# Optimization experiments

Measured on AMD Instinct MI355X. Metric: run time of the kernel, lower is better.

The kernel has to match this reference:

```python
import jax, jax.numpy as jnp
import numpy as np
from jax import lax

TOPK = 10
THRESHOLD = 0.5
MARGIN = 0.5
EPS = 1e-8


def setup_inputs() -> dict:
    key = jax.random.key(0)
    k1, k2 = jax.random.split(key)
    B, C, H, W = 8, 256, 128, 128
    loc_features = jax.random.normal(k1, (B, C, H, W), dtype=jnp.float32)
    det_features = jax.random.normal(k2, (B, C, H, W), dtype=jnp.float32)
    return {"loc_features": loc_features, "det_features": det_features}


def _peak_features(fmap):
    """fmap: [C,H,W] -> (feats [TOPK,C], valid [TOPK] bool).
    Peaks = pixels equal to their 3x3 local max with intensity > THRESHOLD,
    sorted by intensity descending, top TOPK (padded with invalid slots)."""
    C, H, W = fmap.shape
    intensity = jnp.sqrt(jnp.sum(fmap * fmap, axis=0))  # [H,W] L2 norm over channels
    pooled = lax.reduce_window(intensity, -jnp.inf, lax.max,
                               (3, 3), (1, 1), 'SAME')
    peak_mask = (intensity == pooled) & (intensity > THRESHOLD)
    masked = jnp.where(peak_mask, intensity, -jnp.inf).reshape(-1)  # [H*W]
    vals, idx = lax.top_k(masked, TOPK)
    valid = jnp.isfinite(vals)  # slots beyond the actual peak count are -inf
    y = idx // W
    x = idx % W
    feats = fmap[:, y, x].T  # [TOPK, C]
    return feats, valid


def _cosine_sim(a, b):
    # a: [Ka,C], b: [Kb,C]; torch.cosine_similarity semantics with eps clamp
    na = jnp.maximum(jnp.linalg.norm(a, axis=-1), EPS)  # [Ka]
    nb = jnp.maximum(jnp.linalg.norm(b, axis=-1), EPS)  # [Kb]
    return (a @ b.T) / (na[:, None] * nb[None, :])


def _per_sample_loss(det_map, loc_map):
    det_f, det_v = _peak_features(det_map)
    loc_f, loc_v = _peak_features(loc_map)
    sim = _cosine_sim(det_f, loc_f)  # [TOPK, TOPK]
    pair_mask = det_v[:, None] & loc_v[None, :]
    n_pairs = jnp.sum(pair_mask)
    loss_sum = jnp.sum(jnp.where(pair_mask, jax.nn.relu(sim - MARGIN), 0.0))
    # torch 'continue' when either side has no peaks -> contributes 0
    return jnp.where(n_pairs > 0, loss_sum / jnp.maximum(n_pairs, 1).astype(sim.dtype), 0.0)


def reference(loc_features, det_features):
    B = loc_features.shape[0]
    losses = jax.vmap(_per_sample_loss)(det_features, loc_features)  # [B]
    return jnp.sum(losses) / B
```

## Files before the change

### kernel.cpp

```cpp
#include <hip/hip_runtime.h>
#include <math.h>

namespace {
constexpr int kB = 8;
constexpr int kC = 256;
constexpr int kH = 128;
constexpr int kW = 128;
constexpr int kHW = kH * kW;
constexpr int kTopK = 10;
constexpr float kThreshold = 0.5f;
constexpr float kMargin = 0.5f;
constexpr float kEps = 1e-8f;
constexpr int kMaps = 2 * kB;
constexpr int kGrpPlanes = 16;
constexpr int kGroups = kC / kGrpPlanes;
constexpr int kQuarter = kHW / 4;
constexpr int kBands = 16;
constexpr int kBandRows = kH / kBands;
}

__global__ __launch_bounds__(512, 4) void sumsq_kernel(
    const float* __restrict__ loc, const float* __restrict__ det,
    float* __restrict__ partial) {
  const int bid = blockIdx.x;
  const int m = bid >> 6;
  const int g = (bid >> 2) & 15;
  const int q = bid & 3;
  const int t = threadIdx.x;
  const float* __restrict__ src = (m < kB) ? loc : det;
  const int b = m & (kB - 1);
  const float* base = src + (size_t)b * kC * kHW +
                      (size_t)(g * kGrpPlanes) * kHW + q * kQuarter + t * 4;
  float4 a0 = {0.f, 0.f, 0.f, 0.f};
  float4 a1 = {0.f, 0.f, 0.f, 0.f};
  for (int j = 0; j < kGrpPlanes; j += 8) {
    float4 v[16];
#pragma unroll
    for (int jj = 0; jj < 8; ++jj) {
      const float* pb = base + (size_t)(j + jj) * kHW;
      v[2 * jj] = *(const float4*)pb;
      v[2 * jj + 1] = *(const float4*)(pb + 2048);
    }
    __builtin_amdgcn_sched_barrier(0);
#pragma unroll
    for (int jj = 0; jj < 8; ++jj) {
      const float4 u = v[2 * jj];
      const float4 x = v[2 * jj + 1];
      a0.x = fmaf(u.x, u.x, a0.x);
      a0.y = fmaf(u.y, u.y, a0.y);
      a0.z = fmaf(u.z, u.z, a0.z);
      a0.w = fmaf(u.w, u.w, a0.w);
      a1.x = fmaf(x.x, x.x, a1.x);
      a1.y = fmaf(x.y, x.y, a1.y);
      a1.z = fmaf(x.z, x.z, a1.z);
      a1.w = fmaf(x.w, x.w, a1.w);
    }
  }
  float* out = partial + ((size_t)m * kGroups + g) * kHW + q * kQuarter + t * 4;
  *(float4*)out = a0;
  *(float4*)(out + 2048) = a1;
}

__global__ __launch_bounds__(256) void peaktop_kernel(
    const float* __restrict__ partial, float* __restrict__ cvals,
    int* __restrict__ cidx) {
  const int m = blockIdx.x >> 4;
  const int band = blockIdx.x & 15;
  const int r0 = band * kBandRows;
  const int t = threadIdx.x;
  const int w = t >> 6;
  const int lane = t & 63;
  __shared__ float ld[kBandRows + 2][kW + 4];
  __shared__ float swv[4][kTopK];
  __shared__ int swi[4][kTopK];

  const int prow0 = r0 - 1;
  float acc[5] = {0.f, 0.f, 0.f, 0.f, 0.f};
  const float* pbase = partial + (size_t)m * kGroups * kHW + prow0 * kW;
#pragma unroll 4
  for (int g = 0; g < kGroups; ++g) {
    const float* pg = pbase + (size_t)g * kHW;
#pragma unroll
    for (int i = 0; i < 5; ++i) {
      const int p = t + 256 * i;
      const int gr = prow0 + (p >> 7);
      if (gr >= 0 && gr < kH) acc[i] += pg[p];
    }
  }
#pragma unroll
  for (int i = 0; i < 5; ++i) {
    const int p = t + 256 * i;
    const int gr = prow0 + (p >> 7);
    ld[p >> 7][p & 127] = (gr >= 0 && gr < kH) ? sqrtf(acc[i]) : -INFINITY;
  }
  __syncthreads();

  float cv[4];
  int ci[4];
#pragma unroll
  for (int i = 0; i < 4; ++i) {
    const int op = t + 256 * i;
    const int tr = (op >> 7) + 1;
    const int col = op & 127;
    const float c0 = ld[tr][col];
    float nmax = -INFINITY;
#pragma unroll
    for (int dy = -1; dy <= 1; ++dy) {
#pragma unroll
      for (int dx = -1; dx <= 1; ++dx) {
        const int xx = col + dx;
        if (xx >= 0 && xx < kW) nmax = fmaxf(nmax, ld[tr + dy][xx]);
      }
    }
    const bool peak = (c0 > kThreshold) && (c0 >= nmax);
    cv[i] = peak ? c0 : -INFINITY;
    ci[i] = (r0 + (op >> 7)) * kW + col;
  }

  for (int r = 0; r < kTopK; ++r) {
    float bv = cv[0];
    int bi = ci[0];
#pragma unroll
    for (int i = 1; i < 4; ++i)
      if (cv[i] > bv || (cv[i] == bv && ci[i] < bi)) { bv = cv[i]; bi = ci[i]; }
    for (int off = 1; off < 64; off <<= 1) {
      const float ov = __shfl_xor(bv, off, 64);
      const int oi = __shfl_xor(bi, off, 64);
      if (ov > bv || (ov == bv && oi < bi)) { bv = ov; bi = oi; }
    }
    if (lane == r) { swv[w][r] = bv; swi[w][r] = bi; }
#pragma unroll
    for (int i = 0; i < 4; ++i)
      if (ci[i] == bi) cv[i] = -INFINITY;
  }
  __syncthreads();

  if (w == 0) {
    float v0 = -INFINITY;
    int i0 = 0x7fffffff;
    if (lane < 4 * kTopK) { v0 = swv[lane / kTopK][lane % kTopK];
                            i0 = swi[lane / kTopK][lane % kTopK]; }
    for (int r = 0; r < kTopK; ++r) {
      float bv = v0;
      int bi = i0;
      for (int off = 1; off < 64; off <<= 1) {
        const float ov = __shfl_xor(bv, off, 64);
        const int oi = __shfl_xor(bi, off, 64);
        if (ov > bv || (ov == bv && oi < bi)) { bv = ov; bi = oi; }
      }
      if (lane == r) {
        cvals[(m * kBands + band) * kTopK + r] = bv;
        cidx[(m * kBands + band) * kTopK + r] = bi;
      }
      if (i0 == bi) { v0 = -INFINITY; i0 = 0x7fffffff; }
    }
  }
}

__global__ __launch_bounds__(64) void merge_kernel(
    const float* __restrict__ cvals, const int* __restrict__ cidx,
    float* __restrict__ tvals, int* __restrict__ tidx) {
  const int m = blockIdx.x;
  const int lane = threadIdx.x;
  float cv[3];
  int ci[3];
#pragma unroll
  for (int q = 0; q < 3; ++q) {
    const int s = lane + 64 * q;
    if (s < kBands * kTopK) {
      cv[q] = cvals[m * kBands * kTopK + s];
      ci[q] = cidx[m * kBands * kTopK + s];
    } else {
      cv[q] = -INFINITY;
      ci[q] = 0x7fffffff;
    }
  }
  for (int r = 0; r < kTopK; ++r) {
    float bv = cv[0];
    int bi = ci[0];
#pragma unroll
    for (int q = 1; q < 3; ++q)
      if (cv[q] > bv || (cv[q] == bv && ci[q] < bi)) { bv = cv[q]; bi = ci[q]; }
    for (int off = 1; off < 64; off <<= 1) {
      const float ov = __shfl_xor(bv, off, 64);
      const int oi = __shfl_xor(bi, off, 64);
      if (ov > bv || (ov == bv && oi < bi)) { bv = ov; bi = oi; }
    }
    if (lane == r) {
      tvals[m * kTopK + r] = bv;
      tidx[m * kTopK + r] = bi;
    }
#pragma unroll
    for (int q = 0; q < 3; ++q)
      if (ci[q] == bi) { cv[q] = -INFINITY; ci[q] = 0x7fffffff; }
  }
}

__global__ __launch_bounds__(256) void loss_kernel(
    const float* __restrict__ loc, const float* __restrict__ det,
    const float* __restrict__ tvals, const int* __restrict__ tidx,
    float* __restrict__ losses) {
  const int b = blockIdx.x;
  const int t = threadIdx.x;
  __shared__ float ds[kTopK][kC + 1];
  __shared__ float ls[kTopK][kC + 1];
  __shared__ float s_red[kC];

  float lv[kTopK], dv[kTopK];
  int li[kTopK], di[kTopK];
#pragma unroll
  for (int i = 0; i < kTopK; ++i) {
    lv[i] = tvals[b * kTopK + i];
    li[i] = tidx[b * kTopK + i];
    dv[i] = tvals[(kB + b) * kTopK + i];
    di[i] = tidx[(kB + b) * kTopK + i];
  }
  const float* lb = loc + (size_t)b * kC * kHW + (size_t)t * kHW;
  const float* db = det + (size_t)b * kC * kHW + (size_t)t * kHW;
#pragma unroll
  for (int i = 0; i < kTopK; ++i) {
    ls[i][t] = lb[li[i]];
    ds[i][t] = db[di[i]];
  }
  __syncthreads();

  float contrib = 0.f;
  if (t < kTopK * kTopK) {
    const int i = t / kTopK;
    const int j = t % kTopK;
    const bool valid = (dv[i] > -1e30f) && (lv[j] > -1e30f);
    if (valid) {
      float dot = 0.f;
#pragma unroll 8
      for (int c = 0; c < kC; ++c) dot = fmaf(ds[i][c], ls[j][c], dot);
      const float na = fmaxf(dv[i], kEps);
      const float nb = fmaxf(lv[j], kEps);
      const float sim = dot / (na * nb);
      contrib = fmaxf(sim - kMargin, 0.f);
    }
  }
  s_red[t] = contrib;
  __syncthreads();
  if (t == 0) {
    int nd = 0, nl = 0;
    for (int i = 0; i < kTopK; ++i) {
      nd += (dv[i] > -1e30f) ? 1 : 0;
      nl += (lv[i] > -1e30f) ? 1 : 0;
    }
    float s = 0.f;
    for (int k = 0; k < kTopK * kTopK; ++k) s += s_red[k];
    const int np = nd * nl;
    losses[b] = (np > 0) ? (s / (float)np) : 0.f;
  }
}

__global__ void final_kernel(const float* __restrict__ losses,
                             float* __restrict__ out) {
  if (threadIdx.x == 0 && blockIdx.x == 0) {
    float s = 0.f;
    for (int i = 0; i < kB; ++i) s += losses[i];
    out[0] = s / (float)kB;
  }
}

extern "C" void kernel_launch(void* const* d_in, const int* in_sizes, int n_in,
                              void* d_out, int out_size, void* d_ws,
                              size_t ws_size, hipStream_t stream) {
  const float* loc = (const float*)d_in[0];
  const float* det = (const float*)d_in[1];
  float* out = (float*)d_out;

  float* wsf = (float*)d_ws;
  float* partial = wsf;
  float* cvals = partial + (size_t)kMaps * kGroups * kHW;
  int* cidx = (int*)(cvals + kMaps * kBands * kTopK);
  float* tvals = (float*)(cidx + kMaps * kBands * kTopK);
  int* tidx = (int*)(tvals + kMaps * kTopK);
  float* losses = (float*)(tidx + kMaps * kTopK);

  sumsq_kernel<<<dim3(kMaps * kGroups * 4), dim3(512), 0, stream>>>(loc, det,
                                                                    partial);
  peaktop_kernel<<<dim3(kMaps * kBands), dim3(256), 0, stream>>>(partial,
                                                                 cvals, cidx);
  merge_kernel<<<dim3(kMaps), dim3(64), 0, stream>>>(cvals, cidx, tvals, tidx);
  loss_kernel<<<dim3(kB), dim3(kC), 0, stream>>>(loc, det, tvals, tidx,
                                                 losses);
  final_kernel<<<dim3(1), dim3(64), 0, stream>>>(losses, out);
}
```

Baseline: 337.5 us.

## Restructure sum-of-squares kernel to one block per plane group with LDS accumulators

The sum-of-squares kernel now assigns each block a full 128x128 plane region for a 16-channel group instead of a quarter. It accumulates per-pixel squares in a 64KB shared-memory array while streaming channels one at a time with nontemporal loads. This cuts the grid fourfold and lowers register pressure, but the 64KB of LDS per block limits occupancy and adds an LDS read and write per channel. The loads are also now issued one plane at a time (8 float4 per thread) rather than as batches spanning 8 planes.

```diff
diff --git a/kernel.cpp b/kernel.cpp
--- a/kernel.cpp
+++ b/kernel.cpp
@@ -14,51 +14,64 @@
 constexpr int kMaps = 2 * kB;
 constexpr int kGrpPlanes = 16;
 constexpr int kGroups = kC / kGrpPlanes;
-constexpr int kQuarter = kHW / 4;
 constexpr int kBands = 16;
 constexpr int kBandRows = kH / kBands;
-}
-
-__global__ __launch_bounds__(512, 4) void sumsq_kernel(
+typedef float vf4 __attribute__((ext_vector_type(4)));
+}
+
+__global__ __launch_bounds__(512) void sumsq_kernel(
     const float* __restrict__ loc, const float* __restrict__ det,
     float* __restrict__ partial) {
+  __shared__ float acc[kHW];
   const int bid = blockIdx.x;
-  const int m = bid >> 6;
-  const int g = (bid >> 2) & 15;
-  const int q = bid & 3;
+  const int m = bid >> 4;
+  const int g = bid & 15;
   const int t = threadIdx.x;
+  const int w = t >> 6;
+  const int lane = t & 63;
   const float* __restrict__ src = (m < kB) ? loc : det;
   const int b = m & (kB - 1);
   const float* base = src + (size_t)b * kC * kHW +
-                      (size_t)(g * kGrpPlanes) * kHW + q * kQuarter + t * 4;
-  float4 a0 = {0.f, 0.f, 0.f, 0.f};
-  float4 a1 = {0.f, 0.f, 0.f, 0.f};
-  for (int j = 0; j < kGrpPlanes; j += 8) {
-    float4 v[16];
-#pragma unroll
-    for (int jj = 0; jj < 8; ++jj) {
-      const float* pb = base + (size_t)(j + jj) * kHW;
-      v[2 * jj] = *(const float4*)pb;
-      v[2 * jj + 1] = *(const float4*)(pb + 2048);
-    }
+                      (size_t)(g * kGrpPlanes) * kHW + w * 2048 + lane * 4;
+  float* lacc = acc + w * 2048 + lane * 4;
+
+  {
+    vf4 v[8];
+#pragma unroll
+    for (int i = 0; i < 8; ++i)
+      v[i] = __builtin_nontemporal_load((const vf4*)(base + i * 256));
     __builtin_amdgcn_sched_barrier(0);
 #pragma unroll
-    for (int jj = 0; jj < 8; ++jj) {
-      const float4 u = v[2 * jj];
-      const float4 x = v[2 * jj + 1];
-      a0.x = fmaf(u.x, u.x, a0.x);
-      a0.y = fmaf(u.y, u.y, a0.y);
-      a0.z = fmaf(u.z, u.z, a0.z);
-      a0.w = fmaf(u.w, u.w, a0.w);
-      a1.x = fmaf(x.x, x.x, a1.x);
-      a1.y = fmaf(x.y, x.y, a1.y);
-      a1.z = fmaf(x.z, x.z, a1.z);
-      a1.w = fmaf(x.w, x.w, a1.w);
-    }
-  }
-  float* out = partial + ((size_t)m * kGroups + g) * kHW + q * kQuarter + t * 4;
-  *(float4*)out = a0;
-  *(float4*)(out + 2048) = a1;
+    for (int i = 0; i < 8; ++i) {
+      vf4 o;
+      o.x = v[i].x * v[i].x;
+      o.y = v[i].y * v[i].y;
+      o.z = v[i].z * v[i].z;
+      o.w = v[i].w * v[i].w;
+      *(vf4*)(lacc + i * 256) = o;
+    }
+  }
+  for (int j = 1; j < kGrpPlanes; ++j) {
+    const float* pb = base + (size_t)j * kHW;
+    vf4 v[8];
+#pragma unroll
+    for (int i = 0; i < 8; ++i)
+      v[i] = __builtin_nontemporal_load((const vf4*)(pb + i * 256));
+    __builtin_amdgcn_sched_barrier(0);
+#pragma unroll
+    for (int i = 0; i < 8; ++i) {
+      vf4 a = *(const vf4*)(lacc + i * 256);
+      a.x = fmaf(v[i].x, v[i].x, a.x);
+      a.y = fmaf(v[i].y, v[i].y, a.y);
+      a.z = fmaf(v[i].z, v[i].z, a.z);
+      a.w = fmaf(v[i].w, v[i].w, a.w);
+      *(vf4*)(lacc + i * 256) = a;
+    }
+  }
+  float* out = partial + ((size_t)m * kGroups + g) * kHW + w * 2048 + lane * 4;
+#pragma unroll
+  for (int i = 0; i < 8; ++i)
+    *(vf4*)(out + i * 256) = *(const vf4*)(lacc + i * 256);
 }
 
 __global__ __launch_bounds__(256) void peaktop_kernel(
@@ -278,8 +291,8 @@
   int* tidx = (int*)(tvals + kMaps * kTopK);
   float* losses = (float*)(tidx + kMaps * kTopK);
 
-  sumsq_kernel<<<dim3(kMaps * kGroups * 4), dim3(512), 0, stream>>>(loc, det,
-                                                                    partial);
+  sumsq_kernel<<<dim3(kMaps * kGroups), dim3(512), 0, stream>>>(loc, det,
+                                                                partial);
   peaktop_kernel<<<dim3(kMaps * kBands), dim3(256), 0, stream>>>(partial,
                                                                  cvals, cidx);
   merge_kernel<<<dim3(kMaps), dim3(64), 0, stream>>>(cvals, cidx, tvals, tidx);
```

Result: faster. 315.1 us (-6.6%).
